# Performance work log

Measured on AMD Instinct MI355X. Metric: run time of the kernel, lower is better.

The kernel has to match this reference:

```python
import jax, jax.numpy as jnp
import numpy as np

N_NODES = 100000
N_EDGES = 3200000
N_FEAT = 512
HIDDEN = 16
N_CLASSES = 40


def gcn_conv(x, src, dst, W, b, num_nodes):
    # GCNConv with self-loops and symmetric normalization (default PyG settings).
    loop = jnp.arange(num_nodes)
    s = jnp.concatenate([src, loop])
    d = jnp.concatenate([dst, loop])
    deg = jax.ops.segment_sum(jnp.ones_like(s, dtype=x.dtype), d, num_segments=num_nodes)
    dinv = jnp.where(deg > 0, jax.lax.rsqrt(deg), 0.0)
    norm = dinv[s] * dinv[d]  # [E+N]
    h = x @ W  # [N, out]
    msg = h[s] * norm[:, None]  # gather + scale
    out = jax.ops.segment_sum(msg, d, num_segments=num_nodes)  # scatter-add
    return out + b


def setup_inputs() -> dict:
    key = jax.random.key(0)
    k1, k2, k3, k4 = jax.random.split(key, 4)
    x = jax.random.normal(k1, (N_NODES, N_FEAT), dtype=jnp.float32)
    edge_index = jax.random.randint(k2, (2, N_EDGES), 0, N_NODES, dtype=jnp.int64)
    W1 = jax.random.normal(k3, (N_FEAT, HIDDEN), dtype=jnp.float32) * 0.05
    b1 = jnp.zeros((HIDDEN,), dtype=jnp.float32)
    W2 = jax.random.normal(k4, (HIDDEN, N_CLASSES), dtype=jnp.float32) * 0.05
    b2 = jnp.zeros((N_CLASSES,), dtype=jnp.float32)
    return {"x": x, "edge_index": edge_index, "W1": W1, "b1": b1, "W2": W2, "b2": b2}


def reference(x, edge_index, W1, b1, W2, b2):
    num_nodes = x.shape[0]
    src, dst = edge_index[0], edge_index[1]
    h = gcn_conv(x, src, dst, W1, b1, num_nodes)
    h = jax.nn.relu(h)
    # dropout is identity in eval mode (training=False)
    out = gcn_conv(h, src, dst, W2, b2, num_nodes)
    return jax.nn.log_softmax(out, axis=1)
```

## Files before the change

kernel.cpp:

```cpp
#include <hip/hip_runtime.h>

#define N_NODES 100000
#define N_EDGES 3200000
#define N_FEAT 512
#define HIDDEN 16
#define N_CLASSES 40

#define SCAN_BLOCKS 98

#define CH    16384
#define NCH   7
#define NS    32
#define SLICE (N_EDGES / NS)
#define SL4   (SLICE / 4)

#define CH3   256
#define NCHK  391
#define NS2   256
#define SLICE2 (N_EDGES / NS2)
#define SL4_2  (SLICE2 / 4)

typedef int v4i __attribute__((ext_vector_type(4)));
typedef int v2i __attribute__((ext_vector_type(2)));

__global__ __launch_bounds__(512) void k_p1(const int* __restrict__ dst,
                                            int* __restrict__ partS) {
    __shared__ int hist[CH];
    int tid = threadIdx.x;
    int s = blockIdx.x, j = blockIdx.y;
    int base = j * CH;
    int lim = N_NODES - base; if (lim > CH) lim = CH;
    for (int i = tid; i < CH; i += 512) hist[i] = 0;
    __syncthreads();
    const v4i* dp = reinterpret_cast<const v4i*>(dst + s * SLICE);
    for (int i = tid; i < SL4; i += 512) {
        v4i d4 = __builtin_nontemporal_load(dp + i);
        unsigned a = (unsigned)(d4.x - base); if (a < (unsigned)lim) atomicAdd(&hist[a], 1);
        unsigned b = (unsigned)(d4.y - base); if (b < (unsigned)lim) atomicAdd(&hist[b], 1);
        unsigned c = (unsigned)(d4.z - base); if (c < (unsigned)lim) atomicAdd(&hist[c], 1);
        unsigned d = (unsigned)(d4.w - base); if (d < (unsigned)lim) atomicAdd(&hist[d], 1);
    }
    __syncthreads();
    for (int i = tid; i < lim; i += 512)
        partS[s * N_NODES + base + i] = hist[i];
}

__global__ __launch_bounds__(256) void k_colscan(const int* __restrict__ partS,
                                                 int* __restrict__ deg,
                                                 float* __restrict__ dinv) {
    int n = blockIdx.x * 256 + threadIdx.x;
    if (n >= N_NODES) return;
    int run = 0;
    #pragma unroll
    for (int s = 0; s < NS; s++) run += partS[s * N_NODES + n];
    deg[n] = run;
    dinv[n] = rsqrtf((float)(run + 1));
}


__global__ __launch_bounds__(1024) void k_scan_a(const int* __restrict__ cnt,
                                                 int* __restrict__ bsum) {
    int tid = threadIdx.x;
    int i = blockIdx.x * 1024 + tid;
    int v = (i < N_NODES) ? cnt[i] : 0;
    #pragma unroll
    for (int off = 32; off >= 1; off >>= 1) v += __shfl_xor(v, off, 64);
    __shared__ int ws[16];
    if ((tid & 63) == 0) ws[tid >> 6] = v;
    __syncthreads();
    if (tid == 0) {
        int s = 0;
        #pragma unroll
        for (int w = 0; w < 16; w++) s += ws[w];
        bsum[blockIdx.x] = s;
    }
}

__global__ __launch_bounds__(128) void k_scan_b(const int* __restrict__ bsum,
                                                int* __restrict__ boff) {
    int tid = threadIdx.x;
    int lane = tid & 63, wv = tid >> 6;
    int v = (tid < SCAN_BLOCKS) ? bsum[tid] : 0;
    int sc = v;
    #pragma unroll
    for (int off = 1; off < 64; off <<= 1) {
        int t = __shfl_up(sc, off, 64);
        if (lane >= off) sc += t;
    }
    __shared__ int wsum[2];
    if (lane == 63) wsum[wv] = sc;
    __syncthreads();
    int pre = (wv == 1) ? wsum[0] : 0;
    if (tid < SCAN_BLOCKS) boff[tid] = pre + sc - v;
}

__global__ __launch_bounds__(1024) void k_scan_c(const int* __restrict__ cnt,
                                                 const int* __restrict__ boff,
                                                 int* __restrict__ row_start) {
    int tid = threadIdx.x;
    int i = blockIdx.x * 1024 + tid;
    int lane = tid & 63, wv = tid >> 6;
    int v = (i < N_NODES) ? cnt[i] : 0;
    int sc = v;
    #pragma unroll
    for (int off = 1; off < 64; off <<= 1) {
        int t = __shfl_up(sc, off, 64);
        if (lane >= off) sc += t;
    }
    __shared__ int wsum[16];
    if (lane == 63) wsum[wv] = sc;
    __syncthreads();
    int pre = 0;
    #pragma unroll
    for (int w = 0; w < 16; w++) pre += (w < wv) ? wsum[w] : 0;
    int excl = boff[blockIdx.x] + pre + sc - v;
    if (i < N_NODES) row_start[i] = excl;
    if (i == N_NODES) row_start[N_NODES] = N_EDGES;
}

__global__ __launch_bounds__(512) void k_p1b(const int* __restrict__ dst,
                                             int* __restrict__ cnt_sc) {
    __shared__ int hist[NCHK];
    int tid = threadIdx.x;
    int s = blockIdx.x;
    for (int i = tid; i < NCHK; i += 512) hist[i] = 0;
    __syncthreads();
    const v4i* dp = reinterpret_cast<const v4i*>(dst + s * SLICE2);
    for (int i = tid; i < SL4_2; i += 512) {
        v4i d4 = __builtin_nontemporal_load(dp + i);
        atomicAdd(&hist[(unsigned)d4.x >> 8], 1);
        atomicAdd(&hist[(unsigned)d4.y >> 8], 1);
        atomicAdd(&hist[(unsigned)d4.z >> 8], 1);
        atomicAdd(&hist[(unsigned)d4.w >> 8], 1);
    }
    __syncthreads();
    for (int i = tid; i < NCHK; i += 512)
        cnt_sc[s * NCHK + i] = hist[i];
}

__global__ __launch_bounds__(512) void k_scstage(const int* __restrict__ cnt_sc,
                                                 int* __restrict__ sbase,
                                                 int* __restrict__ cb) {
    int tid = threadIdx.x;
    int tot = 0;
    if (tid < NCHK) {
        int run = 0;
        #pragma unroll 8
        for (int s = 0; s < NS2; s++) {
            int v = cnt_sc[s * NCHK + tid];
            sbase[s * NCHK + tid] = run;
            run += v;
        }
        tot = run;
    }
    int lane = tid & 63, wv = tid >> 6;
    int sc = tot;
    #pragma unroll
    for (int off = 1; off < 64; off <<= 1) {
        int t = __shfl_up(sc, off, 64);
        if (lane >= off) sc += t;
    }
    __shared__ int wsum[8];
    if (lane == 63) wsum[wv] = sc;
    __syncthreads();
    int pre = 0;
    #pragma unroll
    for (int w = 0; w < 8; w++) pre += (w < wv) ? wsum[w] : 0;
    int excl = pre + sc - tot;
    if (tid < NCHK) cb[tid] = excl;
    if (tid == NCHK - 1) cb[NCHK] = excl + tot;
}

__global__ __launch_bounds__(512) void k_p2stage(const int* __restrict__ src,
                                                 const int* __restrict__ dst,
                                                 const int* __restrict__ sbase,
                                                 const int* __restrict__ cb,
                                                 int2* __restrict__ staged) {
    __shared__ int curpos[NCHK];
    int tid = threadIdx.x;
    int s = blockIdx.x;
    for (int c = tid; c < NCHK; c += 512)
        curpos[c] = cb[c] + sbase[s * NCHK + c];
    __syncthreads();
    const v4i* dp = reinterpret_cast<const v4i*>(dst + s * SLICE2);
    const v4i* sp = reinterpret_cast<const v4i*>(src + s * SLICE2);
    for (int i = tid; i < SL4_2; i += 512) {
        v4i d4 = __builtin_nontemporal_load(dp + i);
        v4i s4 = __builtin_nontemporal_load(sp + i);
        int p0 = atomicAdd(&curpos[(unsigned)d4.x >> 8], 1);
        staged[p0] = make_int2(s4.x, d4.x);
        int p1 = atomicAdd(&curpos[(unsigned)d4.y >> 8], 1);
        staged[p1] = make_int2(s4.y, d4.y);
        int p2 = atomicAdd(&curpos[(unsigned)d4.z >> 8], 1);
        staged[p2] = make_int2(s4.z, d4.z);
        int p3 = atomicAdd(&curpos[(unsigned)d4.w >> 8], 1);
        staged[p3] = make_int2(s4.w, d4.w);
    }
}

__global__ __launch_bounds__(512) void k_p3(const int2* __restrict__ staged,
                                            const int* __restrict__ cb,
                                            const int* __restrict__ row_start,
                                            const float* __restrict__ dinv,
                                            int2* __restrict__ edge_data) {
    __shared__ int cur[CH3];
    __shared__ float dv[CH3];
    int tid = threadIdx.x;
    int c = blockIdx.x;
    int base = c << 8;
    int lim = N_NODES - base; if (lim > CH3) lim = CH3;
    if (tid < lim) {
        cur[tid] = row_start[base + tid];
        dv[tid]  = dinv[base + tid];
    }
    __syncthreads();
    int beg = cb[c], end = cb[c + 1];
    const v2i* stp = reinterpret_cast<const v2i*>(staged);
    for (int i = beg + tid; i < end; i += 512) {
        v2i e = __builtin_nontemporal_load(stp + i);
        int nl = e.y - base;
        float nrm = dinv[e.x] * dv[nl];
        int slot = atomicAdd(&cur[nl], 1);
        edge_data[slot] = make_int2(e.x, __float_as_int(nrm));
    }
}


#define KC 32
#define LDSW 36

__global__ __launch_bounds__(256) void k_gemm1(const float* __restrict__ x,
                                               const float* __restrict__ W1,
                                               float* __restrict__ h1) {
    __shared__ float xs[256 * LDSW];
    int tid = threadIdx.x;
    int row = blockIdx.x * 256 + tid;

    float acc[HIDDEN];
    #pragma unroll
    for (int j = 0; j < HIDDEN; j++) acc[j] = 0.f;

    int s_sub = tid >> 3;
    int s_k4  = tid & 7;

    for (int kc = 0; kc < N_FEAT; kc += KC) {
        __syncthreads();
        #pragma unroll
        for (int l = 0; l < 8; l++) {
            int srow = s_sub + l * 32;
            int grow = blockIdx.x * 256 + srow;
            int gr = grow < N_NODES ? grow : N_NODES - 1;
            float4 v = *reinterpret_cast<const float4*>(
                x + (size_t)gr * N_FEAT + kc + s_k4 * 4);
            *reinterpret_cast<float4*>(&xs[srow * LDSW + s_k4 * 4]) = v;
        }
        __syncthreads();

        const float* Wc = W1 + kc * HIDDEN;
        #pragma unroll
        for (int k4 = 0; k4 < 8; k4++) {
            float4 xv = *reinterpret_cast<const float4*>(&xs[tid * LDSW + k4 * 4]);
            const float* w0 = Wc + (k4 * 4 + 0) * HIDDEN;
            const float* w1 = Wc + (k4 * 4 + 1) * HIDDEN;
            const float* w2 = Wc + (k4 * 4 + 2) * HIDDEN;
            const float* w3 = Wc + (k4 * 4 + 3) * HIDDEN;
            #pragma unroll
            for (int j = 0; j < HIDDEN; j++) {
                acc[j] += xv.x * w0[j];
                acc[j] += xv.y * w1[j];
                acc[j] += xv.z * w2[j];
                acc[j] += xv.w * w3[j];
            }
        }
    }

    if (row < N_NODES) {
        float4* op = reinterpret_cast<float4*>(h1 + (size_t)row * HIDDEN);
        #pragma unroll
        for (int q = 0; q < 4; q++)
            op[q] = make_float4(acc[q*4+0], acc[q*4+1], acc[q*4+2], acc[q*4+3]);
    }
}


template <bool RELU>
__global__ __launch_bounds__(256) void k_agg16(const int2* __restrict__ edge_data,
                                               const int* __restrict__ row_start,
                                               const float* __restrict__ dinv,
                                               const float* __restrict__ h,
                                               const float* __restrict__ bias,
                                               float* __restrict__ out) {
    int g = threadIdx.x >> 4, j = threadIdx.x & 15;
    int node = blockIdx.x * 16 + g;
    if (node >= N_NODES) return;
    int beg = row_start[node], end = row_start[node + 1];
    float ds = dinv[node];
    float acc = h[(size_t)node * HIDDEN + j] * (ds * ds);
    int i = beg;
    for (; i + 3 < end; i += 4) {
        int2 e0 = edge_data[i + 0];
        int2 e1 = edge_data[i + 1];
        int2 e2 = edge_data[i + 2];
        int2 e3 = edge_data[i + 3];
        float v0 = h[(size_t)e0.x * HIDDEN + j];
        float v1 = h[(size_t)e1.x * HIDDEN + j];
        float v2 = h[(size_t)e2.x * HIDDEN + j];
        float v3 = h[(size_t)e3.x * HIDDEN + j];
        acc += v0 * __int_as_float(e0.y);
        acc += v1 * __int_as_float(e1.y);
        acc += v2 * __int_as_float(e2.y);
        acc += v3 * __int_as_float(e3.y);
    }
    for (; i < end; ++i) {
        int2 ed = edge_data[i];
        acc += h[(size_t)ed.x * HIDDEN + j] * __int_as_float(ed.y);
    }
    if (RELU) acc = fmaxf(acc + bias[j], 0.f);
    out[(size_t)node * HIDDEN + j] = acc;
}


__global__ __launch_bounds__(256) void k_out(const float* __restrict__ agg2,
                                             const float* __restrict__ W2,
                                             const float* __restrict__ b2,
                                             float* __restrict__ out) {
    int r = blockIdx.x * 256 + threadIdx.x;
    if (r >= N_NODES) return;
    float a[HIDDEN];
    const float4* ap = reinterpret_cast<const float4*>(agg2 + (size_t)r * HIDDEN);
    #pragma unroll
    for (int q = 0; q < 4; q++) {
        float4 v = ap[q];
        a[q * 4 + 0] = v.x; a[q * 4 + 1] = v.y;
        a[q * 4 + 2] = v.z; a[q * 4 + 3] = v.w;
    }
    float acc[N_CLASSES];
    #pragma unroll
    for (int jj = 0; jj < N_CLASSES; jj++) acc[jj] = b2[jj];
    #pragma unroll
    for (int kk = 0; kk < HIDDEN; kk++) {
        float av = a[kk];
        #pragma unroll
        for (int jj = 0; jj < N_CLASSES; jj++)
            acc[jj] += av * W2[kk * N_CLASSES + jj];
    }
    float m = -1e30f;
    #pragma unroll
    for (int jj = 0; jj < N_CLASSES; jj++) m = fmaxf(m, acc[jj]);
    float sum = 0.f;
    #pragma unroll
    for (int jj = 0; jj < N_CLASSES; jj++) sum += __expf(acc[jj] - m);
    float l = m + __logf(sum);
    float4* op = reinterpret_cast<float4*>(out + (size_t)r * N_CLASSES);
    #pragma unroll
    for (int q = 0; q < N_CLASSES / 4; q++) {
        op[q] = make_float4(acc[q*4+0] - l, acc[q*4+1] - l,
                            acc[q*4+2] - l, acc[q*4+3] - l);
    }
}


extern "C" void kernel_launch(void* const* d_in, const int* in_sizes, int n_in,
                              void* d_out, int out_size, void* d_ws, size_t ws_size,
                              hipStream_t stream) {
    const float* x  = (const float*)d_in[0];
    const int*   ei = (const int*)d_in[1];
    const float* W1 = (const float*)d_in[2];
    const float* b1 = (const float*)d_in[3];
    const float* W2 = (const float*)d_in[4];
    const float* b2 = (const float*)d_in[5];
    const int* src = ei;
    const int* dst = ei + N_EDGES;
    float* out = (float*)d_out;

    char* ws = (char*)d_ws;
    size_t off = 0;
    auto alloc = [&](size_t bytes) {
        size_t o = off; off = (off + bytes + 255) & ~(size_t)255; return o;
    };
    float* dinv      = (float*)(ws + alloc(sizeof(float) * N_NODES));
    int*   cnt       = (int*)  (ws + alloc(sizeof(int) * N_NODES));
    int*   row_start = (int*)  (ws + alloc(sizeof(int) * (N_NODES + 1)));
    int*   cnt_sc    = (int*)  (ws + alloc(sizeof(int) * NS2 * NCHK));
    int*   sbase     = (int*)  (ws + alloc(sizeof(int) * NS2 * NCHK));
    int*   cb        = (int*)  (ws + alloc(sizeof(int) * (NCHK + 1)));
    int*   partS     = (int*)  (ws + alloc(sizeof(int) * (size_t)NS * N_NODES));
    float* h1        = (float*)(ws + alloc(sizeof(float) * N_NODES * HIDDEN));
    float* rbuf      = (float*)(ws + alloc(sizeof(float) * N_NODES * HIDDEN));
    int2*  staged    = (int2*)partS;
    int2*  edge_data = (int2*) (ws + alloc(sizeof(int2) * N_EDGES));
    float* agg2      = (float*)(ws + alloc(sizeof(float) * N_NODES * HIDDEN));
    int*   bsum      = (int*)  (ws + alloc(sizeof(int) * SCAN_BLOCKS));
    int*   boff      = (int*)  (ws + alloc(sizeof(int) * SCAN_BLOCKS));

    const int nodeBlocks  = (N_NODES + 255) / 256;
    const int aggBlocks   = (N_NODES + 15) / 16;

    k_p1<<<dim3(NS, NCH), 512, 0, stream>>>(dst, partS);
    k_p1b<<<NS2, 512, 0, stream>>>(dst, cnt_sc);
    k_colscan<<<nodeBlocks, 256, 0, stream>>>(partS, cnt, dinv);
    k_scan_a<<<SCAN_BLOCKS, 1024, 0, stream>>>(cnt, bsum);
    k_scan_b<<<1, 128, 0, stream>>>(bsum, boff);
    k_scan_c<<<SCAN_BLOCKS, 1024, 0, stream>>>(cnt, boff, row_start);
    k_scstage<<<1, 512, 0, stream>>>(cnt_sc, sbase, cb);
    k_p2stage<<<NS2, 512, 0, stream>>>(src, dst, sbase, cb, staged);
    k_p3<<<NCHK, 512, 0, stream>>>(staged, cb, row_start, dinv, edge_data);

    k_gemm1<<<nodeBlocks, 256, 0, stream>>>(x, W1, h1);
    k_agg16<true><<<aggBlocks, 256, 0, stream>>>(edge_data, row_start, dinv, h1, b1, rbuf);
    k_agg16<false><<<aggBlocks, 256, 0, stream>>>(edge_data, row_start, dinv, rbuf, nullptr, agg2);
    k_out<<<nodeBlocks, 256, 0, stream>>>(agg2, W2, b2, out);
}
```

Before: 581.9 us.

## Derive degrees from staged buckets, parallelize stage scan, use 64-lane aggregation

Drops the separate 32-slice by 7-chunk degree histogram pass (k_p1 plus k_colscan) and computes per-node degree from the already bucketed staged edges in a per-chunk LDS count kernel. The single-block sequential slice scan becomes a wave-parallel scan over chunks plus a small scan of chunk totals. Aggregation now assigns one 64-lane wave per node, with four sub-groups splitting the edges and a shuffle reduction at the end, to raise memory-level parallelism. The workspace layout is reshuffled so h1 and rbuf alias the staged buffer, which is only valid if staged is dead before gemm1 runs.

```diff
diff --git a/kernel.cpp b/kernel.cpp
--- a/kernel.cpp
+++ b/kernel.cpp
@@ -8,12 +8,6 @@
 
 #define SCAN_BLOCKS 98
 
-#define CH    16384
-#define NCH   7
-#define NS    32
-#define SLICE (N_EDGES / NS)
-#define SL4   (SLICE / 4)
-
 #define CH3   256
 #define NCHK  391
 #define NS2   256
@@ -22,101 +16,6 @@
 
 typedef int v4i __attribute__((ext_vector_type(4)));
 typedef int v2i __attribute__((ext_vector_type(2)));
-
-__global__ __launch_bounds__(512) void k_p1(const int* __restrict__ dst,
-                                            int* __restrict__ partS) {
-    __shared__ int hist[CH];
-    int tid = threadIdx.x;
-    int s = blockIdx.x, j = blockIdx.y;
-    int base = j * CH;
-    int lim = N_NODES - base; if (lim > CH) lim = CH;
-    for (int i = tid; i < CH; i += 512) hist[i] = 0;
-    __syncthreads();
-    const v4i* dp = reinterpret_cast<const v4i*>(dst + s * SLICE);
-    for (int i = tid; i < SL4; i += 512) {
-        v4i d4 = __builtin_nontemporal_load(dp + i);
-        unsigned a = (unsigned)(d4.x - base); if (a < (unsigned)lim) atomicAdd(&hist[a], 1);
-        unsigned b = (unsigned)(d4.y - base); if (b < (unsigned)lim) atomicAdd(&hist[b], 1);
-        unsigned c = (unsigned)(d4.z - base); if (c < (unsigned)lim) atomicAdd(&hist[c], 1);
-        unsigned d = (unsigned)(d4.w - base); if (d < (unsigned)lim) atomicAdd(&hist[d], 1);
-    }
-    __syncthreads();
-    for (int i = tid; i < lim; i += 512)
-        partS[s * N_NODES + base + i] = hist[i];
-}
-
-__global__ __launch_bounds__(256) void k_colscan(const int* __restrict__ partS,
-                                                 int* __restrict__ deg,
-                                                 float* __restrict__ dinv) {
-    int n = blockIdx.x * 256 + threadIdx.x;
-    if (n >= N_NODES) return;
-    int run = 0;
-    #pragma unroll
-    for (int s = 0; s < NS; s++) run += partS[s * N_NODES + n];
-    deg[n] = run;
-    dinv[n] = rsqrtf((float)(run + 1));
-}
-
-
-__global__ __launch_bounds__(1024) void k_scan_a(const int* __restrict__ cnt,
-                                                 int* __restrict__ bsum) {
-    int tid = threadIdx.x;
-    int i = blockIdx.x * 1024 + tid;
-    int v = (i < N_NODES) ? cnt[i] : 0;
-    #pragma unroll
-    for (int off = 32; off >= 1; off >>= 1) v += __shfl_xor(v, off, 64);
-    __shared__ int ws[16];
-    if ((tid & 63) == 0) ws[tid >> 6] = v;
-    __syncthreads();
-    if (tid == 0) {
-        int s = 0;
-        #pragma unroll
-        for (int w = 0; w < 16; w++) s += ws[w];
-        bsum[blockIdx.x] = s;
-    }
-}
-
-__global__ __launch_bounds__(128) void k_scan_b(const int* __restrict__ bsum,
-                                                int* __restrict__ boff) {
-    int tid = threadIdx.x;
-    int lane = tid & 63, wv = tid >> 6;
-    int v = (tid < SCAN_BLOCKS) ? bsum[tid] : 0;
-    int sc = v;
-    #pragma unroll
-    for (int off = 1; off < 64; off <<= 1) {
-        int t = __shfl_up(sc, off, 64);
-        if (lane >= off) sc += t;
-    }
-    __shared__ int wsum[2];
-    if (lane == 63) wsum[wv] = sc;
-    __syncthreads();
-    int pre = (wv == 1) ? wsum[0] : 0;
-    if (tid < SCAN_BLOCKS) boff[tid] = pre + sc - v;
-}
-
-__global__ __launch_bounds__(1024) void k_scan_c(const int* __restrict__ cnt,
-                                                 const int* __restrict__ boff,
-                                                 int* __restrict__ row_start) {
-    int tid = threadIdx.x;
-    int i = blockIdx.x * 1024 + tid;
-    int lane = tid & 63, wv = tid >> 6;
-    int v = (i < N_NODES) ? cnt[i] : 0;
-    int sc = v;
-    #pragma unroll
-    for (int off = 1; off < 64; off <<= 1) {
-        int t = __shfl_up(sc, off, 64);
-        if (lane >= off) sc += t;
-    }
-    __shared__ int wsum[16];
-    if (lane == 63) wsum[wv] = sc;
-    __syncthreads();
-    int pre = 0;
-    #pragma unroll
-    for (int w = 0; w < 16; w++) pre += (w < wv) ? wsum[w] : 0;
-    int excl = boff[blockIdx.x] + pre + sc - v;
-    if (i < N_NODES) row_start[i] = excl;
-    if (i == N_NODES) row_start[N_NODES] = N_EDGES;
-}
 
 __global__ __launch_bounds__(512) void k_p1b(const int* __restrict__ dst,
                                              int* __restrict__ cnt_sc) {
@@ -138,23 +37,35 @@
         cnt_sc[s * NCHK + i] = hist[i];
 }
 
-__global__ __launch_bounds__(512) void k_scstage(const int* __restrict__ cnt_sc,
-                                                 int* __restrict__ sbase,
-                                                 int* __restrict__ cb) {
-    int tid = threadIdx.x;
-    int tot = 0;
-    if (tid < NCHK) {
-        int run = 0;
-        #pragma unroll 8
-        for (int s = 0; s < NS2; s++) {
-            int v = cnt_sc[s * NCHK + tid];
-            sbase[s * NCHK + tid] = run;
-            run += v;
+__global__ __launch_bounds__(256) void k_scstage2(const int* __restrict__ cnt_sc,
+                                                  int* __restrict__ sbase,
+                                                  int* __restrict__ tot) {
+    int c = blockIdx.x * 4 + (threadIdx.x >> 6);
+    int lane = threadIdx.x & 63;
+    if (c >= NCHK) return;
+    int carry = 0;
+    #pragma unroll
+    for (int r = 0; r < 4; r++) {
+        int s = r * 64 + lane;
+        int v = cnt_sc[s * NCHK + c];
+        int sc = v;
+        #pragma unroll
+        for (int off = 1; off < 64; off <<= 1) {
+            int t = __shfl_up(sc, off, 64);
+            if (lane >= off) sc += t;
         }
-        tot = run;
-    }
+        sbase[s * NCHK + c] = carry + sc - v;
+        carry += __shfl(sc, 63, 64);
+    }
+    if (lane == 0) tot[c] = carry;
+}
+
+__global__ __launch_bounds__(512) void k_cbscan(const int* __restrict__ tot,
+                                                int* __restrict__ cb) {
+    int tid = threadIdx.x;
+    int v = (tid < NCHK) ? tot[tid] : 0;
     int lane = tid & 63, wv = tid >> 6;
-    int sc = tot;
+    int sc = v;
     #pragma unroll
     for (int off = 1; off < 64; off <<= 1) {
         int t = __shfl_up(sc, off, 64);
@@ -166,9 +77,9 @@
     int pre = 0;
     #pragma unroll
     for (int w = 0; w < 8; w++) pre += (w < wv) ? wsum[w] : 0;
-    int excl = pre + sc - tot;
+    int excl = pre + sc - v;
     if (tid < NCHK) cb[tid] = excl;
-    if (tid == NCHK - 1) cb[NCHK] = excl + tot;
+    if (tid == NCHK - 1) cb[NCHK] = excl + v;
 }
 
 __global__ __launch_bounds__(512) void k_p2stage(const int* __restrict__ src,
@@ -196,6 +107,92 @@
         int p3 = atomicAdd(&curpos[(unsigned)d4.w >> 8], 1);
         staged[p3] = make_int2(s4.w, d4.w);
     }
+}
+
+__global__ __launch_bounds__(256) void k_deg(const int2* __restrict__ staged,
+                                             const int* __restrict__ cb,
+                                             int* __restrict__ deg,
+                                             float* __restrict__ dinv) {
+    __shared__ int cnt[CH3];
+    int tid = threadIdx.x;
+    int c = blockIdx.x;
+    int base = c << 8;
+    int lim = N_NODES - base; if (lim > CH3) lim = CH3;
+    cnt[tid] = 0;
+    __syncthreads();
+    int beg = cb[c], end = cb[c + 1];
+    const v2i* stp = reinterpret_cast<const v2i*>(staged);
+    for (int i = beg + tid; i < end; i += 256) {
+        v2i e = stp[i];
+        atomicAdd(&cnt[e.y - base], 1);
+    }
+    __syncthreads();
+    if (tid < lim) {
+        int d = cnt[tid];
+        deg[base + tid] = d;
+        dinv[base + tid] = rsqrtf((float)(d + 1));
+    }
+}
+
+
+__global__ __launch_bounds__(1024) void k_scan_a(const int* __restrict__ cnt,
+                                                 int* __restrict__ bsum) {
+    int tid = threadIdx.x;
+    int i = blockIdx.x * 1024 + tid;
+    int v = (i < N_NODES) ? cnt[i] : 0;
+    #pragma unroll
+    for (int off = 32; off >= 1; off >>= 1) v += __shfl_xor(v, off, 64);
+    __shared__ int ws[16];
+    if ((tid & 63) == 0) ws[tid >> 6] = v;
+    __syncthreads();
+    if (tid == 0) {
+        int s = 0;
+        #pragma unroll
+        for (int w = 0; w < 16; w++) s += ws[w];
+        bsum[blockIdx.x] = s;
+    }
+}
+
+__global__ __launch_bounds__(128) void k_scan_b(const int* __restrict__ bsum,
+                                                int* __restrict__ boff) {
+    int tid = threadIdx.x;
+    int lane = tid & 63, wv = tid >> 6;
+    int v = (tid < SCAN_BLOCKS) ? bsum[tid] : 0;
+    int sc = v;
+    #pragma unroll
+    for (int off = 1; off < 64; off <<= 1) {
+        int t = __shfl_up(sc, off, 64);
+        if (lane >= off) sc += t;
+    }
+    __shared__ int wsum[2];
+    if (lane == 63) wsum[wv] = sc;
+    __syncthreads();
+    int pre = (wv == 1) ? wsum[0] : 0;
+    if (tid < SCAN_BLOCKS) boff[tid] = pre + sc - v;
+}
+
+__global__ __launch_bounds__(1024) void k_scan_c(const int* __restrict__ cnt,
+                                                 const int* __restrict__ boff,
+                                                 int* __restrict__ row_start) {
+    int tid = threadIdx.x;
+    int i = blockIdx.x * 1024 + tid;
+    int lane = tid & 63, wv = tid >> 6;
+    int v = (i < N_NODES) ? cnt[i] : 0;
+    int sc = v;
+    #pragma unroll
+    for (int off = 1; off < 64; off <<= 1) {
+        int t = __shfl_up(sc, off, 64);
+        if (lane >= off) sc += t;
+    }
+    __shared__ int wsum[16];
+    if (lane == 63) wsum[wv] = sc;
+    __syncthreads();
+    int pre = 0;
+    #pragma unroll
+    for (int w = 0; w < 16; w++) pre += (w < wv) ? wsum[w] : 0;
+    int excl = boff[blockIdx.x] + pre + sc - v;
+    if (i < N_NODES) row_start[i] = excl;
+    if (i == N_NODES) row_start[N_NODES] = N_EDGES;
 }
 
 __global__ __launch_bounds__(512) void k_p3(const int2* __restrict__ staged,
@@ -284,39 +281,43 @@
 
 
 template <bool RELU>
-__global__ __launch_bounds__(256) void k_agg16(const int2* __restrict__ edge_data,
-                                               const int* __restrict__ row_start,
-                                               const float* __restrict__ dinv,
-                                               const float* __restrict__ h,
-                                               const float* __restrict__ bias,
-                                               float* __restrict__ out) {
-    int g = threadIdx.x >> 4, j = threadIdx.x & 15;
-    int node = blockIdx.x * 16 + g;
-    if (node >= N_NODES) return;
+__global__ __launch_bounds__(256) void k_aggw(const int2* __restrict__ edge_data,
+                                              const int* __restrict__ row_start,
+                                              const float* __restrict__ dinv,
+                                              const float* __restrict__ h,
+                                              const float* __restrict__ bias,
+                                              float* __restrict__ out) {
+    int lane = threadIdx.x & 63;
+    int node = blockIdx.x * 4 + (threadIdx.x >> 6);
+    int sub = lane >> 4, j = lane & 15;
     int beg = row_start[node], end = row_start[node + 1];
     float ds = dinv[node];
-    float acc = h[(size_t)node * HIDDEN + j] * (ds * ds);
-    int i = beg;
-    for (; i + 3 < end; i += 4) {
-        int2 e0 = edge_data[i + 0];
-        int2 e1 = edge_data[i + 1];
-        int2 e2 = edge_data[i + 2];
-        int2 e3 = edge_data[i + 3];
-        float v0 = h[(size_t)e0.x * HIDDEN + j];
-        float v1 = h[(size_t)e1.x * HIDDEN + j];
-        float v2 = h[(size_t)e2.x * HIDDEN + j];
-        float v3 = h[(size_t)e3.x * HIDDEN + j];
-        acc += v0 * __int_as_float(e0.y);
-        acc += v1 * __int_as_float(e1.y);
-        acc += v2 * __int_as_float(e2.y);
-        acc += v3 * __int_as_float(e3.y);
-    }
-    for (; i < end; ++i) {
-        int2 ed = edge_data[i];
-        acc += h[(size_t)ed.x * HIDDEN + j] * __int_as_float(ed.y);
-    }
-    if (RELU) acc = fmaxf(acc + bias[j], 0.f);
-    out[(size_t)node * HIDDEN + j] = acc;
+    float acc = (sub == 0) ? h[(size_t)node * HIDDEN + j] * (ds * ds) : 0.f;
+    int i = beg + sub;
+    for (; i + 12 < end; i += 16) {
+        int2 ea = edge_data[i];
+        int2 eb = edge_data[i + 4];
+        int2 ec = edge_data[i + 8];
+        int2 ed = edge_data[i + 12];
+        float va = h[(size_t)ea.x * HIDDEN + j];
+        float vb = h[(size_t)eb.x * HIDDEN + j];
+        float vc = h[(size_t)ec.x * HIDDEN + j];
+        float vd = h[(size_t)ed.x * HIDDEN + j];
+        acc += va * __int_as_float(ea.y);
+        acc += vb * __int_as_float(eb.y);
+        acc += vc * __int_as_float(ec.y);
+        acc += vd * __int_as_float(ed.y);
+    }
+    for (; i < end; i += 4) {
+        int2 e = edge_data[i];
+        acc += h[(size_t)e.x * HIDDEN + j] * __int_as_float(e.y);
+    }
+    acc += __shfl_xor(acc, 16, 64);
+    acc += __shfl_xor(acc, 32, 64);
+    if (sub == 0) {
+        if (RELU) acc = fmaxf(acc + bias[j], 0.f);
+        out[(size_t)node * HIDDEN + j] = acc;
+    }
 }
 
 
@@ -384,30 +385,30 @@
     int*   cnt_sc    = (int*)  (ws + alloc(sizeof(int) * NS2 * NCHK));
     int*   sbase     = (int*)  (ws + alloc(sizeof(int) * NS2 * NCHK));
     int*   cb        = (int*)  (ws + alloc(sizeof(int) * (NCHK + 1)));
-    int*   partS     = (int*)  (ws + alloc(sizeof(int) * (size_t)NS * N_NODES));
-    float* h1        = (float*)(ws + alloc(sizeof(float) * N_NODES * HIDDEN));
-    float* rbuf      = (float*)(ws + alloc(sizeof(float) * N_NODES * HIDDEN));
-    int2*  staged    = (int2*)partS;
+    int*   tot       = (int*)  (ws + alloc(sizeof(int) * NCHK));
+    int2*  staged    = (int2*) (ws + alloc(sizeof(int2) * N_EDGES));
+    float* h1        = (float*)(ws + off - (size_t)N_EDGES * sizeof(int2));
+    float* rbuf      = h1 + (size_t)N_NODES * HIDDEN;
     int2*  edge_data = (int2*) (ws + alloc(sizeof(int2) * N_EDGES));
     float* agg2      = (float*)(ws + alloc(sizeof(float) * N_NODES * HIDDEN));
     int*   bsum      = (int*)  (ws + alloc(sizeof(int) * SCAN_BLOCKS));
     int*   boff      = (int*)  (ws + alloc(sizeof(int) * SCAN_BLOCKS));
 
-    const int nodeBlocks  = (N_NODES + 255) / 256;
-    const int aggBlocks   = (N_NODES + 15) / 16;
-
-    k_p1<<<dim3(NS, NCH), 512, 0, stream>>>(dst, partS);
+    const int nodeBlocks = (N_NODES + 255) / 256;
+    const int aggBlocks  = N_NODES / 4;
+
     k_p1b<<<NS2, 512, 0, stream>>>(dst, cnt_sc);
-    k_colscan<<<nodeBlocks, 256, 0, stream>>>(partS, cnt, dinv);
+    k_scstage2<<<(NCHK + 3) / 4, 256, 0, stream>>>(cnt_sc, sbase, tot);
+    k_cbscan<<<1, 512, 0, stream>>>(tot, cb);
+    k_p2stage<<<NS2, 512, 0, stream>>>(src, dst, sbase, cb, staged);
+    k_deg<<<NCHK, 256, 0, stream>>>(staged, cb, cnt, dinv);
     k_scan_a<<<SCAN_BLOCKS, 1024, 0, stream>>>(cnt, bsum);
     k_scan_b<<<1, 128, 0, stream>>>(bsum, boff);
     k_scan_c<<<SCAN_BLOCKS, 1024, 0, stream>>>(cnt, boff, row_start);
-    k_scstage<<<1, 512, 0, stream>>>(cnt_sc, sbase, cb);
-    k_p2stage<<<NS2, 512, 0, stream>>>(src, dst, sbase, cb, staged);
     k_p3<<<NCHK, 512, 0, stream>>>(staged, cb, row_start, dinv, edge_data);
 
     k_gemm1<<<nodeBlocks, 256, 0, stream>>>(x, W1, h1);
-    k_agg16<true><<<aggBlocks, 256, 0, stream>>>(edge_data, row_start, dinv, h1, b1, rbuf);
-    k_agg16<false><<<aggBlocks, 256, 0, stream>>>(edge_data, row_start, dinv, rbuf, nullptr, agg2);
+    k_aggw<true><<<aggBlocks, 256, 0, stream>>>(edge_data, row_start, dinv, h1, b1, rbuf);
+    k_aggw<false><<<aggBlocks, 256, 0, stream>>>(edge_data, row_start, dinv, rbuf, nullptr, agg2);
     k_out<<<nodeBlocks, 256, 0, stream>>>(agg2, W2, b2, out);
 }
```

New measurement: 571.0 us. About the same (-1.9%).
